# Optimization experiments

Hardware: AMD Instinct MI355X
Metric: run time of the kernel (lower is better)

Reference implementation:

```python
import jax, jax.numpy as jnp
import numpy as np

N = 50000          # nodes
E = 800000         # edges (avg degree 16)
IN, H, OUT = 128, 256, 128
K = 100            # low-rank attention rank (hard-coded self.k = 100)
BN_EPS = 1e-5


def _lin(key, din, dout):
    return jax.random.normal(key, (din, dout), jnp.float32) / np.sqrt(din)


def setup_inputs() -> dict:
    key = jax.random.key(0)
    ks = jax.random.split(key, 16)
    inp = {
        "x": jax.random.normal(ks[0], (N, IN), jnp.float32),
        "edge_index": jax.random.randint(ks[1], (2, E), 0, N, jnp.int32),
    }
    dins = [IN, H, H]
    douts = [H, H, OUT]
    j = 2
    for i, (di, do) in enumerate(zip(dins, douts)):
        inp[f"cw{i}"] = _lin(ks[j], di, H); j += 1          # GCNConv weight
        inp[f"cb{i}"] = jnp.zeros((H,), jnp.float32)          # GCNConv bias
        inp[f"aw{i}"] = _lin(ks[j], di, 4 * K); j += 1        # attention U|V|Z|T projection
        inp[f"ab{i}"] = jnp.zeros((4 * K,), jnp.float32)
        inp[f"rw{i}"] = _lin(ks[j], 2 * K + H, do); j += 1    # dimension_reduce linear
        inp[f"rb{i}"] = jnp.zeros((do,), jnp.float32)
    for i in range(2):                                        # BN for first num_layers-1 blocks
        inp[f"g{i}"] = jnp.ones((H,), jnp.float32)
        inp[f"bt{i}"] = jnp.zeros((H,), jnp.float32)
    return inp


def _gcn(x, W, b, src, dst):
    n = x.shape[0]
    loops = jnp.arange(n, dtype=src.dtype)
    s = jnp.concatenate([src, loops])
    d = jnp.concatenate([dst, loops])
    deg = jax.ops.segment_sum(jnp.ones(d.shape, x.dtype), d, num_segments=n)
    dis = jax.lax.rsqrt(jnp.maximum(deg, 1.0))  # deg >= 1 due to self loops
    h = x @ W                                    # [N, H]
    msg = h[s] * (dis[s] * dis[d])[:, None]      # [E+N, H]
    return jax.ops.segment_sum(msg, d, num_segments=n) + b


def _lowrank(x, Aw, Ab):
    # LowRankAttention: tmp = relu(x W); split into U,V,Z,T of width K each.
    t = jax.nn.relu(x @ Aw + Ab)                 # [N, 4K]
    U, V, Z, T = t[:, :K], t[:, K:2 * K], t[:, 2 * K:3 * K], t[:, 3 * K:]
    n = x.shape[0]
    # joint_normalize2: scalar norm factor
    nf = jnp.sum(U @ (V.T @ jnp.ones((n, 1), x.dtype))) / n + 1e-6
    res = U @ (V.T @ Z)                          # low-rank global attention [N, K]
    return jnp.concatenate([res / nf, T], axis=1)  # [N, 2K]


def _bn(x, g, b):
    m = jnp.mean(x, axis=0)
    v = jnp.var(x, axis=0)
    return (x - m) * jax.lax.rsqrt(v + BN_EPS) * g + b


def reference(x, edge_index, cw0, cb0, aw0, ab0, rw0, rb0, g0, bt0,
              cw1, cb1, aw1, ab1, rw1, rb1, g1, bt1,
              cw2, cb2, aw2, ab2, rw2, rb2):
    src, dst = edge_index[0], edge_index[1]
    layers = [(cw0, cb0, aw0, ab0, rw0, rb0, g0, bt0),
              (cw1, cb1, aw1, ab1, rw1, rb1, g1, bt1)]
    for cw, cb, aw, ab, rw, rb, g, bt in layers:
        x_local = jax.nn.relu(_gcn(x, cw, cb, src, dst))  # dropout p=0 (eval)
        x_global = _lowrank(x, aw, ab)
        x = jax.nn.relu(jnp.concatenate([x_global, x_local], axis=1) @ rw + rb)
        x = _bn(x, g, bt)
    x_local = jax.nn.relu(_gcn(x, cw2, cb2, src, dst))
    x_global = _lowrank(x, aw2, ab2)
    return jnp.concatenate([x_global, x_local], axis=1) @ rw2 + rb2
```

## Files before the change

### kernel.cpp

```cpp
#include <hip/hip_runtime.h>

typedef _Float16 f16;
typedef __attribute__((ext_vector_type(8))) _Float16 f16x8;
typedef __attribute__((ext_vector_type(4))) _Float16 f16x4;
typedef __attribute__((ext_vector_type(2))) _Float16 f16x2;
typedef __attribute__((ext_vector_type(4))) float f32x4;

#define BKMAX 256
#define LDB   264

__global__ __launch_bounds__(256, 2) void gemm_fused3(
    const f16* __restrict__ A, int lda,
    const f16* __restrict__ Bt, int Kd,
    const float* __restrict__ biascat,
    f16* __restrict__ hb, f16* __restrict__ tbuf, f16* __restrict__ xcatT,
    int R, float* __restrict__ csbuf)
{
    __shared__ f16 Bs[128 * LDB];
    const int tid  = threadIdx.x;
    const int wid  = tid >> 6;
    const int lane = tid & 63;
    const int m    = lane & 15;
    const int quad = lane >> 4;

    const long row0    = (long)blockIdx.x * 256 + wid * 64;
    const int  colbase = blockIdx.y * 128;

    f32x4 acc[4][8];
#pragma unroll
    for (int rt = 0; rt < 4; ++rt)
#pragma unroll
        for (int ct = 0; ct < 8; ++ct)
            acc[rt][ct] = f32x4{0.f, 0.f, 0.f, 0.f};

    const f16* Aptr[4];
#pragma unroll
    for (int rt = 0; rt < 4; ++rt) {
        long r = row0 + rt * 16 + m;
        if (r > (long)R - 1) r = (long)R - 1;
        Aptr[rt] = A + r * (long)lda + quad * 8;
    }
    f16x8 pa[4];
#pragma unroll
    for (int rt = 0; rt < 4; ++rt) pa[rt] = *(const f16x8*)(Aptr[rt]);

    const int  scol  = tid >> 1;
    const int  shalf = (tid & 1) * 8;
    const long sbase = (long)(colbase + scol) * Kd;

    for (int k0 = 0; k0 < Kd; k0 += BKMAX) {
        const int BK = (Kd - k0 < BKMAX) ? (Kd - k0) : BKMAX;
        if (k0 != 0) __syncthreads();
        for (int kc = shalf; kc < BK; kc += 16)
            *(f16x8*)&Bs[scol * LDB + kc] = *(const f16x8*)(Bt + sbase + k0 + kc);
        __syncthreads();
#pragma unroll 2
        for (int kk = 0; kk < BK; kk += 32) {
            f16x8 a[4];
#pragma unroll
            for (int rt = 0; rt < 4; ++rt) a[rt] = pa[rt];
            int kn = k0 + kk + 32;
            if (kn < Kd) {
#pragma unroll
                for (int rt = 0; rt < 4; ++rt) pa[rt] = *(const f16x8*)(Aptr[rt] + kn);
            }
#pragma unroll
            for (int ct = 0; ct < 8; ++ct) {
                f16x8 b = *(const f16x8*)&Bs[(ct * 16 + m) * LDB + kk + quad * 8];
#pragma unroll
                for (int rt = 0; rt < 4; ++rt)
                    acc[rt][ct] = __builtin_amdgcn_mfma_f32_16x16x32_f16(a[rt], b, acc[rt][ct], 0, 0, 0);
            }
        }
    }

    float rsum[8];
#pragma unroll
    for (int ct = 0; ct < 8; ++ct) rsum[ct] = 0.f;

#pragma unroll
    for (int ct = 0; ct < 8; ++ct) {
        int col = colbase + ct * 16 + m;
        if (col >= 656) continue;
        float bv = biascat[col];
        bool isrelu = col >= 256;
        f16* dst; int ldc2, c2;
        if (col < 256)      { dst = hb;    ldc2 = 256; c2 = col; }
        else if (col < 556) { dst = tbuf;  ldc2 = 300; c2 = col - 256; }
        else                { dst = xcatT; ldc2 = 456; c2 = col - 556; }
#pragma unroll
        for (int rt = 0; rt < 4; ++rt) {
#pragma unroll
            for (int r = 0; r < 4; ++r) {
                long row = row0 + rt * 16 + quad * 4 + r;
                if (row < R) {
                    float v = acc[rt][ct][r] + bv;
                    if (isrelu && v < 0.f) v = 0.f;
                    dst[row * (long)ldc2 + c2] = (f16)v;
                    rsum[ct] += v;
                }
            }
        }
    }

    if (colbase == 256 || colbase == 384) {
        __syncthreads();
        float* scr = (float*)Bs;
#pragma unroll
        for (int ct = 0; ct < 8; ++ct) {
            float s = rsum[ct];
            s += __shfl_xor(s, 16);
            s += __shfl_xor(s, 32);
            if (quad == 0) scr[wid * 128 + ct * 16 + m] = s;
        }
        __syncthreads();
        if (tid < 128) {
            int gcol = colbase + tid;
            if (gcol < 456) {
                float s = scr[tid] + scr[128 + tid] + scr[256 + tid] + scr[384 + tid];
                atomicAdd(&csbuf[gcol - 256], s);
            }
        }
    }
}

__global__ __launch_bounds__(256) void gemm_mfma(
    const f16* __restrict__ A, int lda,
    const f16* __restrict__ Bt, int Kd,
    const float* __restrict__ bias,
    f16* __restrict__ Cb, float* __restrict__ Cf, int ldc,
    int R, int ncols, int relu,
    const float* __restrict__ scale_ptr)
{
    __shared__ f16 Bs[128 * LDB];
    const int tid  = threadIdx.x;
    const int wid  = tid >> 6;
    const int lane = tid & 63;
    const int m    = lane & 15;
    const int quad = lane >> 4;

    const long row0    = (long)blockIdx.x * 128 + wid * 32;
    const int  colbase = blockIdx.y * 128;

    f32x4 acc[2][8];
#pragma unroll
    for (int rt = 0; rt < 2; ++rt)
#pragma unroll
        for (int ct = 0; ct < 8; ++ct)
            acc[rt][ct] = f32x4{0.f, 0.f, 0.f, 0.f};

    const f16* Aptr[2];
#pragma unroll
    for (int rt = 0; rt < 2; ++rt) {
        long r = row0 + rt * 16 + m;
        if (r > (long)R - 1) r = (long)R - 1;
        Aptr[rt] = A + r * (long)lda + quad * 8;
    }
    f16x8 pa0 = *(const f16x8*)(Aptr[0]);
    f16x8 pa1 = *(const f16x8*)(Aptr[1]);

    const int  scol  = tid >> 1;
    const int  shalf = (tid & 1) * 8;
    const long sbase = (long)(colbase + scol) * Kd;

    for (int k0 = 0; k0 < Kd; k0 += BKMAX) {
        const int BK = (Kd - k0 < BKMAX) ? (Kd - k0) : BKMAX;
        if (k0 != 0) __syncthreads();
        for (int kc = shalf; kc < BK; kc += 16)
            *(f16x8*)&Bs[scol * LDB + kc] = *(const f16x8*)(Bt + sbase + k0 + kc);
        __syncthreads();
#pragma unroll 2
        for (int kk = 0; kk < BK; kk += 32) {
            f16x8 a0 = pa0, a1 = pa1;
            int kn = k0 + kk + 32;
            if (kn < Kd) {
                pa0 = *(const f16x8*)(Aptr[0] + kn);
                pa1 = *(const f16x8*)(Aptr[1] + kn);
            }
#pragma unroll
            for (int ct = 0; ct < 8; ++ct) {
                f16x8 b = *(const f16x8*)&Bs[(ct * 16 + m) * LDB + kk + quad * 8];
                acc[0][ct] = __builtin_amdgcn_mfma_f32_16x16x32_f16(a0, b, acc[0][ct], 0, 0, 0);
                acc[1][ct] = __builtin_amdgcn_mfma_f32_16x16x32_f16(a1, b, acc[1][ct], 0, 0, 0);
            }
        }
    }

    const float scale = scale_ptr ? *scale_ptr : 1.f;
#pragma unroll
    for (int ct = 0; ct < 8; ++ct) {
        int col = colbase + ct * 16 + m;
        if (col >= ncols) continue;
        float bv = bias ? bias[col] : 0.f;
#pragma unroll
        for (int rt = 0; rt < 2; ++rt) {
#pragma unroll
            for (int r = 0; r < 4; ++r) {
                long row = row0 + rt * 16 + quad * 4 + r;
                if (row < R) {
                    float v = acc[rt][ct][r] * scale + bv;
                    if (relu && v < 0.f) v = 0.f;
                    if (Cf) Cf[row * (long)ldc + col] = v;
                    else    Cb[row * (long)ldc + col] = (f16)v;
                }
            }
        }
    }
}

__global__ __launch_bounds__(256, 2) void gemm_mfma_t(
    const f16* __restrict__ A, int lda,
    const f16* __restrict__ Bt, int Kd,
    const float* __restrict__ bias,
    f16* __restrict__ Cb, float* __restrict__ Cf, int ldc,
    int R, int ncols, int relu,
    float* __restrict__ bnsum_ptr)
{
    __shared__ f16 Bs[128 * LDB];
    const int tid  = threadIdx.x;
    const int wid  = tid >> 6;
    const int lane = tid & 63;
    const int m    = lane & 15;
    const int quad = lane >> 4;

    const long row0    = (long)blockIdx.x * 256 + wid * 64;
    const int  colbase = blockIdx.y * 128;

    f32x4 acc[4][8];
#pragma unroll
    for (int rt = 0; rt < 4; ++rt)
#pragma unroll
        for (int ct = 0; ct < 8; ++ct)
            acc[rt][ct] = f32x4{0.f, 0.f, 0.f, 0.f};

    const f16* Aptr[4];
#pragma unroll
    for (int rt = 0; rt < 4; ++rt) {
        long r = row0 + rt * 16 + m;
        if (r > (long)R - 1) r = (long)R - 1;
        Aptr[rt] = A + r * (long)lda + quad * 8;
    }
    f16x8 pa[4];
#pragma unroll
    for (int rt = 0; rt < 4; ++rt) pa[rt] = *(const f16x8*)(Aptr[rt]);

    const int  scol  = tid >> 1;
    const int  shalf = (tid & 1) * 8;
    const long sbase = (long)(colbase + scol) * Kd;

    for (int k0 = 0; k0 < Kd; k0 += BKMAX) {
        const int BK = (Kd - k0 < BKMAX) ? (Kd - k0) : BKMAX;
        if (k0 != 0) __syncthreads();
        for (int kc = shalf; kc < BK; kc += 16)
            *(f16x8*)&Bs[scol * LDB + kc] = *(const f16x8*)(Bt + sbase + k0 + kc);
        __syncthreads();
#pragma unroll 2
        for (int kk = 0; kk < BK; kk += 32) {
            f16x8 a[4];
#pragma unroll
            for (int rt = 0; rt < 4; ++rt) a[rt] = pa[rt];
            int kn = k0 + kk + 32;
            if (kn < Kd) {
#pragma unroll
                for (int rt = 0; rt < 4; ++rt) pa[rt] = *(const f16x8*)(Aptr[rt] + kn);
            }
#pragma unroll
            for (int ct = 0; ct < 8; ++ct) {
                f16x8 b = *(const f16x8*)&Bs[(ct * 16 + m) * LDB + kk + quad * 8];
#pragma unroll
                for (int rt = 0; rt < 4; ++rt)
                    acc[rt][ct] = __builtin_amdgcn_mfma_f32_16x16x32_f16(a[rt], b, acc[rt][ct], 0, 0, 0);
            }
        }
    }

    float rsum[8], rsq[8];
#pragma unroll
    for (int ct = 0; ct < 8; ++ct) { rsum[ct] = 0.f; rsq[ct] = 0.f; }

#pragma unroll
    for (int ct = 0; ct < 8; ++ct) {
        int col = colbase + ct * 16 + m;
        if (col >= ncols) continue;
        float bv = bias ? bias[col] : 0.f;
#pragma unroll
        for (int rt = 0; rt < 4; ++rt) {
#pragma unroll
            for (int r = 0; r < 4; ++r) {
                long row = row0 + rt * 16 + quad * 4 + r;
                if (row < R) {
                    float v = acc[rt][ct][r] + bv;
                    if (relu && v < 0.f) v = 0.f;
                    if (Cf) Cf[row * (long)ldc + col] = v;
                    else    Cb[row * (long)ldc + col] = (f16)v;
                    rsum[ct] += v;
                    rsq[ct]  += v * v;
                }
            }
        }
    }

    if (bnsum_ptr) {
        __syncthreads();
        float* scr = (float*)Bs;
#pragma unroll
        for (int ct = 0; ct < 8; ++ct) {
            float s = rsum[ct];
            s += __shfl_xor(s, 16);
            s += __shfl_xor(s, 32);
            float q = rsq[ct];
            q += __shfl_xor(q, 16);
            q += __shfl_xor(q, 32);
            if (quad == 0) {
                scr[wid * 128 + ct * 16 + m]       = s;
                scr[512 + wid * 128 + ct * 16 + m] = q;
            }
        }
        __syncthreads();
        if (tid < 128) {
            int col = colbase + tid;
            if (col < ncols) {
                float s = scr[tid] + scr[128 + tid] + scr[256 + tid] + scr[384 + tid];
                float q = scr[512 + tid] + scr[640 + tid] + scr[768 + tid] + scr[896 + tid];
                atomicAdd(&bnsum_ptr[col], s);
                atomicAdd(&bnsum_ptr[256 + col], q);
            }
        }
    }
}

struct PrepJobs {
    const float* src[13];
    void*        dst[13];
    int   K[13], ncols[13], Kd[13], type[13];
    long  start[13], elems[13];
    int   njobs;
};

__global__ __launch_bounds__(256) void prep_all(PrepJobs J)
{
    long b = blockIdx.x;
    int j = 0;
    for (int i = 1; i < J.njobs; ++i)
        if (b >= J.start[i]) j = i;
    long idx = (b - J.start[j]) * 256 + threadIdx.x;
    if (idx >= J.elems[j]) return;
    int ty = J.type[j];
    if (ty == 0) {
        int Kd = J.Kd[j];
        int k = (int)(idx % Kd);
        long n = idx / Kd;
        float v = (k < J.K[j] && n < J.ncols[j]) ? J.src[j][(long)k * J.ncols[j] + n] : 0.f;
        ((f16*)J.dst[j])[idx] = (f16)v;
    } else if (ty == 1) {
        ((f16*)J.dst[j])[idx] = (f16)J.src[j][idx];
    } else if (ty == 2) {
        ((float*)J.dst[j])[idx] = 0.f;
    } else {
        float v = (idx >= 256 && idx < 656) ? J.src[j][idx - 256] : 0.f;
        ((float*)J.dst[j])[idx] = v;
    }
}

__global__ void hist_kernel(const int* __restrict__ dst, int E, int* __restrict__ cnt)
{
    int e = blockIdx.x * 256 + threadIdx.x;
    if (e < E) atomicAdd(&cnt[dst[e]], 1);
}

__global__ __launch_bounds__(1024) void scanA_kernel(const int* __restrict__ cnt, int n,
                                                     int* __restrict__ csum)
{
    __shared__ int sdata[1024];
    int t = threadIdx.x;
    int i = blockIdx.x * 1024 + t;
    sdata[t] = (i < n) ? cnt[i] : 0;
    __syncthreads();
    for (int d = 512; d > 0; d >>= 1) {
        if (t < d) sdata[t] += sdata[t + d];
        __syncthreads();
    }
    if (t == 0) csum[blockIdx.x] = sdata[0];
}

__global__ void scanB_kernel(int* __restrict__ csum, int nchunks, int n, int* __restrict__ rowptr)
{
    if (threadIdx.x == 0) {
        int run = 0;
        for (int b = 0; b < nchunks; ++b) {
            int v = csum[b];
            csum[b] = run;
            run += v;
        }
        rowptr[n] = run;
    }
}

__global__ __launch_bounds__(1024) void scanC_kernel(const int* __restrict__ cnt, int n,
                                                     const int* __restrict__ csum,
                                                     int* __restrict__ rowptr,
                                                     int* __restrict__ cursor,
                                                     float* __restrict__ dis)
{
    __shared__ int sdata[1024];
    int t = threadIdx.x;
    int i = blockIdx.x * 1024 + t;
    int v = (i < n) ? cnt[i] : 0;
    sdata[t] = v;
    __syncthreads();
    for (int d = 1; d < 1024; d <<= 1) {
        int x = (t >= d) ? sdata[t - d] : 0;
        __syncthreads();
        sdata[t] += x;
        __syncthreads();
    }
    if (i < n) {
        int excl = csum[blockIdx.x] + sdata[t] - v;
        rowptr[i] = excl;
        cursor[i] = excl;
        dis[i] = rsqrtf((float)(v + 1));
    }
}

__global__ void scatter_kernel(const int* __restrict__ src, const int* __restrict__ dst,
                               int E, int* __restrict__ cursor, int* __restrict__ colidx)
{
    int e = blockIdx.x * 256 + threadIdx.x;
    if (e < E) {
        int d = dst[e];
        int pos = atomicAdd(&cursor[d], 1);
        colidx[pos] = src[e];
    }
}

__global__ __launch_bounds__(256) void agg_kernel(
    const f16* __restrict__ h, const int* __restrict__ rowptr,
    const int* __restrict__ colidx, const float* __restrict__ dis,
    const float* __restrict__ cb, f16* __restrict__ out, int ldc, int R)
{
    int wid = threadIdx.x >> 6, lane = threadIdx.x & 63;
    int i = blockIdx.x * 4 + wid;
    if (i >= R) return;
    float disi = dis[i];
    f16x4 hv = *(const f16x4*)(h + (long)i * 256 + lane * 4);
    float acc[4];
#pragma unroll
    for (int j = 0; j < 4; ++j) acc[j] = (float)hv[j] * disi;
    int e0 = rowptr[i], e1 = rowptr[i + 1];
    int e = e0;
    for (; e + 3 < e1; e += 4) {
        int s0 = colidx[e], s1 = colidx[e + 1], s2 = colidx[e + 2], s3 = colidx[e + 3];
        float w0 = dis[s0], w1 = dis[s1], w2 = dis[s2], w3 = dis[s3];
        f16x4 h0 = *(const f16x4*)(h + (long)s0 * 256 + lane * 4);
        f16x4 h1 = *(const f16x4*)(h + (long)s1 * 256 + lane * 4);
        f16x4 h2 = *(const f16x4*)(h + (long)s2 * 256 + lane * 4);
        f16x4 h3 = *(const f16x4*)(h + (long)s3 * 256 + lane * 4);
#pragma unroll
        for (int j = 0; j < 4; ++j)
            acc[j] += (float)h0[j] * w0 + (float)h1[j] * w1
                    + (float)h2[j] * w2 + (float)h3[j] * w3;
    }
    for (; e < e1; ++e) {
        int s = colidx[e];
        float w = dis[s];
        f16x4 hs = *(const f16x4*)(h + (long)s * 256 + lane * 4);
#pragma unroll
        for (int j = 0; j < 4; ++j) acc[j] += (float)hs[j] * w;
    }
    f16x4 o;
#pragma unroll
    for (int j = 0; j < 4; ++j) {
        float v = acc[j] * disi + cb[lane * 4 + j];
        if (v < 0.f) v = 0.f;
        o[j] = (f16)v;
    }
    *(f16x4*)(out + (long)i * ldc + lane * 4) = o;
}

#define VTZ_BLOCKS 192
__global__ __launch_bounds__(256) void vtz_mfma(const f16* __restrict__ t, int ld, int R,
                                                float* __restrict__ Mpart)
{
    __shared__ f16 Vt[112 * 72];
    __shared__ f16 Zt[112 * 72];
    const int tid  = threadIdx.x;
    const int wid  = tid >> 6;
    const int lane = tid & 63;
    const int m    = lane & 15;
    const int quad = lane >> 4;

    for (int idx = tid; idx < 12 * 64; idx += 256) {
        int c = 100 + (idx >> 6), r = idx & 63;
        Vt[c * 72 + r] = (f16)0.f;
        Zt[c * 72 + r] = (f16)0.f;
    }

    f32x4 acc[2][7];
#pragma unroll
    for (int rt = 0; rt < 2; ++rt)
#pragma unroll
        for (int ct = 0; ct < 7; ++ct)
            acc[rt][ct] = f32x4{0.f, 0.f, 0.f, 0.f};

    for (long base = (long)blockIdx.x * 64; base < R; base += (long)gridDim.x * 64) {
        __syncthreads();
        for (int idx = tid; idx < 50 * 64; idx += 256) {
            int r = idx / 50, c2 = (idx - r * 50) * 2;
            f16x2 v2 = f16x2{(f16)0.f, (f16)0.f};
            f16x2 z2 = f16x2{(f16)0.f, (f16)0.f};
            if (base + r < R) {
                v2 = *(const f16x2*)(t + (base + r) * ld + 100 + c2);
                z2 = *(const f16x2*)(t + (base + r) * ld + 200 + c2);
            }
            Vt[c2 * 72 + r] = v2[0]; Vt[(c2 + 1) * 72 + r] = v2[1];
            Zt[c2 * 72 + r] = z2[0]; Zt[(c2 + 1) * 72 + r] = z2[1];
        }
        __syncthreads();
#pragma unroll
        for (int ks = 0; ks < 2; ++ks) {
            int k0 = ks * 32 + quad * 8;
            f16x8 b[7];
#pragma unroll
            for (int ct = 0; ct < 7; ++ct)
                b[ct] = *(const f16x8*)&Zt[(ct * 16 + m) * 72 + k0];
#pragma unroll
            for (int rt = 0; rt < 2; ++rt) {
                int tr = wid + rt * 4;
                if (tr >= 7) continue;
                f16x8 a = *(const f16x8*)&Vt[(tr * 16 + m) * 72 + k0];
#pragma unroll
                for (int ct = 0; ct < 7; ++ct)
                    acc[rt][ct] = __builtin_amdgcn_mfma_f32_16x16x32_f16(a, b[ct], acc[rt][ct], 0, 0, 0);
            }
        }
    }

    float* out = Mpart + (long)blockIdx.x * 10000;
#pragma unroll
    for (int rt = 0; rt < 2; ++rt) {
        int tr = wid + rt * 4;
        if (tr >= 7) continue;
#pragma unroll
        for (int ct = 0; ct < 7; ++ct) {
            int b = ct * 16 + m;
            if (b >= 100) continue;
#pragma unroll
            for (int r = 0; r < 4; ++r) {
                int a = tr * 16 + quad * 4 + r;
                if (a < 100) out[a * 100 + b] = acc[rt][ct][r];
            }
        }
    }
}

__global__ __launch_bounds__(256) void vtz_reduce2(const float* __restrict__ Mpart,
                                                   f16* __restrict__ MT,
                                                   const float* __restrict__ cs, int R)
{
    __shared__ float s2[256];
    int t = threadIdx.x;
    float v = (t < 100) ? cs[t] * cs[100 + t] : 0.f;
    s2[t] = v;
    __syncthreads();
    for (int d = 128; d > 0; d >>= 1) {
        if (t < d) s2[t] += s2[t + d];
        __syncthreads();
    }
    float scale = 1.0f / (s2[0] / (float)R + 1e-6f);

    int idx = blockIdx.x * 256 + t;
    if (idx >= 10000) return;
    float s = 0.f;
    for (int b = 0; b < VTZ_BLOCKS; ++b) s += Mpart[(long)b * 10000 + idx];
    s *= scale;
    int a = idx / 100, c = idx - a * 100;
    MT[c * 128 + a] = (f16)s;
}

__global__ __launch_bounds__(256) void bn_fold2(
    f16* __restrict__ bigBT,
    const float* __restrict__ cwf, const float* __restrict__ awf,
    const float* __restrict__ bnsum, const float* __restrict__ g,
    const float* __restrict__ bt, int R,
    const float* __restrict__ ab0, float* __restrict__ biascat)
{
    __shared__ float a_s[256], b_s[256];
    const int t = threadIdx.x;
    {
        float s0 = bnsum[t];
        float s1 = bnsum[256 + t];
        float mean = s0 / (float)R;
        float var  = s1 / (float)R - mean * mean;
        if (var < 0.f) var = 0.f;
        float a = g[t] * rsqrtf(var + 1e-5f);
        a_s[t] = a;
        b_s[t] = bt[t] - mean * a;
    }
    __syncthreads();
    const int bid = blockIdx.x;
    if (bid < 768) {
        long idx = (long)bid * 256 + t;
        bigBT[idx] = (f16)((float)bigBT[idx] * a_s[t]);
    } else if (bid == 768) {
        float s = 0.f;
        for (int k = 0; k < 256; ++k) s += b_s[k] * cwf[(long)k * 256 + t];
        biascat[t] = s;
    } else {
        int n = (bid - 769) * 256 + t;
        if (n < 400) {
            float s = ab0[n];
            for (int k = 0; k < 256; ++k) s += b_s[k] * awf[(long)k * 400 + n];
            biascat[256 + n] = s;
        }
    }
}

extern "C" void kernel_launch(void* const* d_in, const int* in_sizes, int n_in,
                              void* d_out, int out_size, void* d_ws, size_t ws_size,
                              hipStream_t stream)
{
    (void)n_in; (void)out_size; (void)ws_size;
    const int N = in_sizes[0] / 128;
    const int E = in_sizes[1] / 2;

    const float* x0 = (const float*)d_in[0];
    const int*  ei   = (const int*)d_in[1];
    const int*  esrc = ei;
    const int*  edst = ei + E;
    const float *cw[3], *cbv[3], *aw[3], *abv[3], *rw[3], *rbv[3];
    for (int l = 0; l < 3; ++l) {
        cw[l]  = (const float*)d_in[2 + 6 * l];
        cbv[l] = (const float*)d_in[3 + 6 * l];
        aw[l]  = (const float*)d_in[4 + 6 * l];
        abv[l] = (const float*)d_in[5 + 6 * l];
        rw[l]  = (const float*)d_in[6 + 6 * l];
        rbv[l] = (const float*)d_in[7 + 6 * l];
    }
    const float* g[2]   = {(const float*)d_in[20], (const float*)d_in[22]};
    const float* btb[2] = {(const float*)d_in[21], (const float*)d_in[23]};

    char* p = (char*)d_ws;
    auto carve = [&](size_t bytes) -> char* {
        char* r = p; p += (bytes + 255) & ~(size_t)255; return r;
    };
    int*   cnt    = (int*)carve((size_t)N * 4);
    int*   rowptr = (int*)carve((size_t)(N + 1) * 4);
    int*   cursor = (int*)carve((size_t)N * 4);
    int*   colidx = (int*)carve((size_t)E * 4);
    float* dis    = (float*)carve((size_t)N * 4);
    int*   csum   = (int*)carve(256 * 4);
    float* Mpart  = (float*)carve((size_t)VTZ_BLOCKS * 10000 * 4);
    float* zr     = (float*)carve(9984 * 4);
    float* csbufL[3] = {zr, zr + 256, zr + 512};
    float* bnsumA = zr + 768;
    float* bnsumB = zr + 1280;
    f16*   MT     = (f16*)(zr + 1792);
    float* biascat = (float*)carve(768 * 4);
    f16*   bigBT[3], *rwT[3];
    int din[3] = {128, 256, 256};
    int dou[3] = {256, 256, 128};
    for (int l = 0; l < 3; ++l) {
        bigBT[l] = (f16*)carve((size_t)768 * din[l] * 2);
        rwT[l]   = (f16*)carve((size_t)dou[l] * 480 * 2);
    }
    f16*   xbf  = (f16*)carve((size_t)N * 256 * 2);
    float* hbuf = (float*)carve((size_t)N * 256 * 4);
    f16*   hb   = (f16*)hbuf;
    f16*   tbuf = (f16*)carve((size_t)N * 300 * 2);
    f16*   xcat = (f16*)carve(((size_t)N * 456 + 32) * 2);

    PrepJobs J{};
    int nj = 0; long blk = 0;
    auto addJob = [&](const float* s, void* d, int K, int nc, int Kd, int ty, long elems) {
        J.src[nj] = s; J.dst[nj] = d; J.K[nj] = K; J.ncols[nj] = nc; J.Kd[nj] = Kd;
        J.type[nj] = ty; J.start[nj] = blk; J.elems[nj] = elems;
        blk += (elems + 255) / 256; ++nj;
    };
    for (int l = 0; l < 3; ++l)
        addJob(cw[l], bigBT[l], din[l], 256, din[l], 0, (long)256 * din[l]);
    for (int l = 0; l < 3; ++l)
        addJob(aw[l], bigBT[l] + (long)256 * din[l], din[l], 400, din[l], 0, (long)512 * din[l]);
    for (int l = 0; l < 3; ++l)
        addJob(rw[l], rwT[l], 456, dou[l], 480, 0, (long)dou[l] * 480);
    addJob(x0, xbf, 0, 0, 0, 1, (long)N * 128);
    addJob(nullptr, zr, 0, 0, 0, 2, 9984);
    addJob(nullptr, cnt, 0, 0, 0, 2, N);
    addJob(abv[0], biascat, 0, 0, 0, 3, 768);
    J.njobs = nj;

    prep_all<<<(unsigned)blk, 256, 0, stream>>>(J);

    const int nchunks = (N + 1023) / 1024;
    hist_kernel<<<(E + 255) / 256, 256, 0, stream>>>(edst, E, cnt);
    scanA_kernel<<<nchunks, 1024, 0, stream>>>(cnt, N, csum);
    scanB_kernel<<<1, 64, 0, stream>>>(csum, nchunks, N, rowptr);
    scanC_kernel<<<nchunks, 1024, 0, stream>>>(cnt, N, csum, rowptr, cursor, dis);
    scatter_kernel<<<(E + 255) / 256, 256, 0, stream>>>(esrc, edst, E, cursor, colidx);

    int lda = 128;
    const unsigned gx  = (unsigned)((N + 127) / 128);
    const unsigned gx2 = (unsigned)((N + 255) / 256);

    for (int l = 0; l < 3; ++l) {
        float* bnsumX = (l == 0) ? bnsumA : bnsumB;

        gemm_fused3<<<dim3(gx2, 6), 256, 0, stream>>>(xbf, lda, bigBT[l], din[l], biascat,
                                                      hb, tbuf, xcat + 100, N, csbufL[l]);
        vtz_mfma<<<VTZ_BLOCKS, 256, 0, stream>>>(tbuf, 300, N, Mpart);
        vtz_reduce2<<<40, 256, 0, stream>>>(Mpart, MT, csbufL[l], N);
        gemm_mfma<<<dim3(gx, 1), 256, 0, stream>>>(tbuf, 300, MT, 128, nullptr,
                                                   xcat, nullptr, 456, N, 100, 0, nullptr);
        agg_kernel<<<(N + 3) / 4, 256, 0, stream>>>(hb, rowptr, colidx, dis, cbv[l],
                                                    xcat + 200, 456, N);
        if (l < 2) {
            gemm_mfma_t<<<dim3(gx2, 2), 256, 0, stream>>>(xcat, 456, rwT[l], 480, rbv[l],
                                                          xbf, nullptr, 256, N, 256, 1,
                                                          bnsumX);
            bn_fold2<<<771, 256, 0, stream>>>(bigBT[l + 1], cw[l + 1], aw[l + 1],
                                              bnsumX, g[l], btb[l], N,
                                              abv[l + 1], biascat);
            lda = 256;
        } else {
            gemm_mfma<<<dim3(gx, 1), 256, 0, stream>>>(xcat, 456, rwT[l], 480, rbv[l],
                                                       nullptr, (float*)d_out, 128, N, 128, 0, nullptr);
        }
    }
}
```

Measured before the change: 957.6 us.

## Unify GEMMs into one kernel staging both A and B tiles in LDS

Replaces three GEMM kernels with a single templated-by-mode kernel that stages 256x64 A tiles and 128x64 B tiles into shared memory per k-step, instead of streaming A directly from global with register prefetch and staging full-K B tiles. The smaller tiles (row stride 72) cut LDS use, which should let two blocks fit per CU, and A rows are now loaded cooperatively and coalesced. The narrow GEMMs also move from 128-row to 256-row tiles. In exchange the global-load prefetch overlap is lost and there are more syncs per K.

Result: slower. 980.2 us (+2.4%).

```diff
diff --git a/kernel.cpp b/kernel.cpp
--- a/kernel.cpp
+++ b/kernel.cpp
@@ -6,24 +6,29 @@
 typedef __attribute__((ext_vector_type(2))) _Float16 f16x2;
 typedef __attribute__((ext_vector_type(4))) float f32x4;
 
-#define BKMAX 256
-#define LDB   264
-
-__global__ __launch_bounds__(256, 2) void gemm_fused3(
+#define LDA2 72
+
+__global__ __launch_bounds__(256, 2) void gemm2(
     const f16* __restrict__ A, int lda,
     const f16* __restrict__ Bt, int Kd,
-    const float* __restrict__ biascat,
-    f16* __restrict__ hb, f16* __restrict__ tbuf, f16* __restrict__ xcatT,
-    int R, float* __restrict__ csbuf)
-{
-    __shared__ f16 Bs[128 * LDB];
+    const float* __restrict__ bias,
+    f16* __restrict__ Cb, float* __restrict__ Cf, int ldc,
+    int R, int ncols, int relu,
+    float* __restrict__ csbuf,
+    float* __restrict__ bnsum_ptr,
+    f16* __restrict__ hbD, f16* __restrict__ tbufD, f16* __restrict__ xcatD,
+    int mode)
+{
+    __shared__ f16 As[256 * LDA2];
+    __shared__ f16 Bs[128 * LDA2];
     const int tid  = threadIdx.x;
     const int wid  = tid >> 6;
     const int lane = tid & 63;
     const int m    = lane & 15;
     const int quad = lane >> 4;
 
-    const long row0    = (long)blockIdx.x * 256 + wid * 64;
+    const long rowblk = (long)blockIdx.x * 256;
+    const long row0   = rowblk + wid * 64;
     const int  colbase = blockIdx.y * 128;
 
     f32x4 acc[4][8];
@@ -33,297 +38,138 @@
         for (int ct = 0; ct < 8; ++ct)
             acc[rt][ct] = f32x4{0.f, 0.f, 0.f, 0.f};
 
-    const f16* Aptr[4];
-#pragma unroll
-    for (int rt = 0; rt < 4; ++rt) {
-        long r = row0 + rt * 16 + m;
-        if (r > (long)R - 1) r = (long)R - 1;
-        Aptr[rt] = A + r * (long)lda + quad * 8;
-    }
-    f16x8 pa[4];
-#pragma unroll
-    for (int rt = 0; rt < 4; ++rt) pa[rt] = *(const f16x8*)(Aptr[rt]);
-
-    const int  scol  = tid >> 1;
-    const int  shalf = (tid & 1) * 8;
-    const long sbase = (long)(colbase + scol) * Kd;
-
-    for (int k0 = 0; k0 < Kd; k0 += BKMAX) {
-        const int BK = (Kd - k0 < BKMAX) ? (Kd - k0) : BKMAX;
-        if (k0 != 0) __syncthreads();
-        for (int kc = shalf; kc < BK; kc += 16)
-            *(f16x8*)&Bs[scol * LDB + kc] = *(const f16x8*)(Bt + sbase + k0 + kc);
+    for (int k0 = 0; k0 < Kd; k0 += 64) {
+        const int BK = (Kd - k0 >= 64) ? 64 : (Kd - k0);
+        const int sb = (BK == 64) ? 3 : 2;
+        const int smask = (1 << sb) - 1;
+        if (k0) __syncthreads();
+        const int itA = BK >> 3;
+        for (int i = 0; i < itA; ++i) {
+            int u = i * 256 + tid;
+            int r = u >> sb, s = u & smask;
+            long rr = rowblk + r; if (rr > (long)R - 1) rr = (long)R - 1;
+            *(f16x8*)&As[r * LDA2 + s * 8] = *(const f16x8*)(A + rr * (long)lda + k0 + s * 8);
+        }
+        const int itB = BK >> 4;
+        for (int i = 0; i < itB; ++i) {
+            int u = i * 256 + tid;
+            int c = u >> sb, s = u & smask;
+            *(f16x8*)&Bs[c * LDA2 + s * 8] =
+                *(const f16x8*)(Bt + (long)(colbase + c) * Kd + k0 + s * 8);
+        }
         __syncthreads();
 #pragma unroll 2
         for (int kk = 0; kk < BK; kk += 32) {
-            f16x8 a[4];
-#pragma unroll
-            for (int rt = 0; rt < 4; ++rt) a[rt] = pa[rt];
-            int kn = k0 + kk + 32;
-            if (kn < Kd) {
-#pragma unroll
-                for (int rt = 0; rt < 4; ++rt) pa[rt] = *(const f16x8*)(Aptr[rt] + kn);
-            }
+            f16x8 a[4], b[8];
+#pragma unroll
+            for (int rt = 0; rt < 4; ++rt)
+                a[rt] = *(const f16x8*)&As[(wid * 64 + rt * 16 + m) * LDA2 + kk + quad * 8];
+#pragma unroll
+            for (int ct = 0; ct < 8; ++ct)
+                b[ct] = *(const f16x8*)&Bs[(ct * 16 + m) * LDA2 + kk + quad * 8];
+#pragma unroll
+            for (int ct = 0; ct < 8; ++ct)
+#pragma unroll
+                for (int rt = 0; rt < 4; ++rt)
+                    acc[rt][ct] = __builtin_amdgcn_mfma_f32_16x16x32_f16(a[rt], b[ct], acc[rt][ct], 0, 0, 0);
+        }
+    }
+
+    float rsum[8], rsq[8];
+#pragma unroll
+    for (int ct = 0; ct < 8; ++ct) { rsum[ct] = 0.f; rsq[ct] = 0.f; }
+
+    if (mode == 1) {
+#pragma unroll
+        for (int ct = 0; ct < 8; ++ct) {
+            int col = colbase + ct * 16 + m;
+            if (col >= 656) continue;
+            float bv = bias[col];
+            bool isrelu = col >= 256;
+            f16* dst; int ldc2, c2;
+            if (col < 256)      { dst = hbD;   ldc2 = 256; c2 = col; }
+            else if (col < 556) { dst = tbufD; ldc2 = 300; c2 = col - 256; }
+            else                { dst = xcatD; ldc2 = 456; c2 = col - 556; }
+#pragma unroll
+            for (int rt = 0; rt < 4; ++rt) {
+#pragma unroll
+                for (int r = 0; r < 4; ++r) {
+                    long row = row0 + rt * 16 + quad * 4 + r;
+                    if (row < R) {
+                        float v = acc[rt][ct][r] + bv;
+                        if (isrelu && v < 0.f) v = 0.f;
+                        dst[row * (long)ldc2 + c2] = (f16)v;
+                        rsum[ct] += v;
+                    }
+                }
+            }
+        }
+        if (colbase == 256 || colbase == 384) {
+            __syncthreads();
+            float* scr = (float*)Bs;
 #pragma unroll
             for (int ct = 0; ct < 8; ++ct) {
-                f16x8 b = *(const f16x8*)&Bs[(ct * 16 + m) * LDB + kk + quad * 8];
-#pragma unroll
-                for (int rt = 0; rt < 4; ++rt)
-                    acc[rt][ct] = __builtin_amdgcn_mfma_f32_16x16x32_f16(a[rt], b, acc[rt][ct], 0, 0, 0);
-            }
-        }
-    }
-
-    float rsum[8];
-#pragma unroll
-    for (int ct = 0; ct < 8; ++ct) rsum[ct] = 0.f;
-
-#pragma unroll
-    for (int ct = 0; ct < 8; ++ct) {
-        int col = colbase + ct * 16 + m;
-        if (col >= 656) continue;
-        float bv = biascat[col];
-        bool isrelu = col >= 256;
-        f16* dst; int ldc2, c2;
-        if (col < 256)      { dst = hb;    ldc2 = 256; c2 = col; }
-        else if (col < 556) { dst = tbuf;  ldc2 = 300; c2 = col - 256; }
-        else                { dst = xcatT; ldc2 = 456; c2 = col - 556; }
-#pragma unroll
-        for (int rt = 0; rt < 4; ++rt) {
-#pragma unroll
-            for (int r = 0; r < 4; ++r) {
-                long row = row0 + rt * 16 + quad * 4 + r;
-                if (row < R) {
-                    float v = acc[rt][ct][r] + bv;
-                    if (isrelu && v < 0.f) v = 0.f;
-                    dst[row * (long)ldc2 + c2] = (f16)v;
-                    rsum[ct] += v;
+                float s = rsum[ct];
+                s += __shfl_xor(s, 16);
+                s += __shfl_xor(s, 32);
+                if (quad == 0) scr[wid * 128 + ct * 16 + m] = s;
+            }
+            __syncthreads();
+            if (tid < 128) {
+                int gcol = colbase + tid;
+                if (gcol < 456) {
+                    float s = scr[tid] + scr[128 + tid] + scr[256 + tid] + scr[384 + tid];
+                    atomicAdd(&csbuf[gcol - 256], s);
                 }
             }
         }
-    }
-
-    if (colbase == 256 || colbase == 384) {
-        __syncthreads();
-        float* scr = (float*)Bs;
+    } else {
 #pragma unroll
         for (int ct = 0; ct < 8; ++ct) {
-            float s = rsum[ct];
-            s += __shfl_xor(s, 16);
-            s += __shfl_xor(s, 32);
-            if (quad == 0) scr[wid * 128 + ct * 16 + m] = s;
-        }
-        __syncthreads();
-        if (tid < 128) {
-            int gcol = colbase + tid;
-            if (gcol < 456) {
-                float s = scr[tid] + scr[128 + tid] + scr[256 + tid] + scr[384 + tid];
-                atomicAdd(&csbuf[gcol - 256], s);
-            }
-        }
-    }
-}
-
-__global__ __launch_bounds__(256) void gemm_mfma(
-    const f16* __restrict__ A, int lda,
-    const f16* __restrict__ Bt, int Kd,
-    const float* __restrict__ bias,
-    f16* __restrict__ Cb, float* __restrict__ Cf, int ldc,
-    int R, int ncols, int relu,
-    const float* __restrict__ scale_ptr)
-{
-    __shared__ f16 Bs[128 * LDB];
-    const int tid  = threadIdx.x;
-    const int wid  = tid >> 6;
-    const int lane = tid & 63;
-    const int m    = lane & 15;
-    const int quad = lane >> 4;
-
-    const long row0    = (long)blockIdx.x * 128 + wid * 32;
-    const int  colbase = blockIdx.y * 128;
-
-    f32x4 acc[2][8];
-#pragma unroll
-    for (int rt = 0; rt < 2; ++rt)
-#pragma unroll
-        for (int ct = 0; ct < 8; ++ct)
-            acc[rt][ct] = f32x4{0.f, 0.f, 0.f, 0.f};
-
-    const f16* Aptr[2];
-#pragma unroll
-    for (int rt = 0; rt < 2; ++rt) {
-        long r = row0 + rt * 16 + m;
-        if (r > (long)R - 1) r = (long)R - 1;
-        Aptr[rt] = A + r * (long)lda + quad * 8;
-    }
-    f16x8 pa0 = *(const f16x8*)(Aptr[0]);
-    f16x8 pa1 = *(const f16x8*)(Aptr[1]);
-
-    const int  scol  = tid >> 1;
-    const int  shalf = (tid & 1) * 8;
-    const long sbase = (long)(colbase + scol) * Kd;
-
-    for (int k0 = 0; k0 < Kd; k0 += BKMAX) {
-        const int BK = (Kd - k0 < BKMAX) ? (Kd - k0) : BKMAX;
-        if (k0 != 0) __syncthreads();
-        for (int kc = shalf; kc < BK; kc += 16)
-            *(f16x8*)&Bs[scol * LDB + kc] = *(const f16x8*)(Bt + sbase + k0 + kc);
-        __syncthreads();
-#pragma unroll 2
-        for (int kk = 0; kk < BK; kk += 32) {
-            f16x8 a0 = pa0, a1 = pa1;
-            int kn = k0 + kk + 32;
-            if (kn < Kd) {
-                pa0 = *(const f16x8*)(Aptr[0] + kn);
-                pa1 = *(const f16x8*)(Aptr[1] + kn);
-            }
+            int col = colbase + ct * 16 + m;
+            if (col >= ncols) continue;
+            float bv = bias ? bias[col] : 0.f;
+#pragma unroll
+            for (int rt = 0; rt < 4; ++rt) {
+#pragma unroll
+                for (int r = 0; r < 4; ++r) {
+                    long row = row0 + rt * 16 + quad * 4 + r;
+                    if (row < R) {
+                        float v = acc[rt][ct][r] + bv;
+                        if (relu && v < 0.f) v = 0.f;
+                        if (Cf) Cf[row * (long)ldc + col] = v;
+                        else    Cb[row * (long)ldc + col] = (f16)v;
+                        rsum[ct] += v;
+                        rsq[ct]  += v * v;
+                    }
+                }
+            }
+        }
+        if (bnsum_ptr) {
+            __syncthreads();
+            float* scr = (float*)Bs;
 #pragma unroll
             for (int ct = 0; ct < 8; ++ct) {
-                f16x8 b = *(const f16x8*)&Bs[(ct * 16 + m) * LDB + kk + quad * 8];
-                acc[0][ct] = __builtin_amdgcn_mfma_f32_16x16x32_f16(a0, b, acc[0][ct], 0, 0, 0);
-                acc[1][ct] = __builtin_amdgcn_mfma_f32_16x16x32_f16(a1, b, acc[1][ct], 0, 0, 0);
-            }
-        }
-    }
-
-    const float scale = scale_ptr ? *scale_ptr : 1.f;
-#pragma unroll
-    for (int ct = 0; ct < 8; ++ct) {
-        int col = colbase + ct * 16 + m;
-        if (col >= ncols) continue;
-        float bv = bias ? bias[col] : 0.f;
-#pragma unroll
-        for (int rt = 0; rt < 2; ++rt) {
-#pragma unroll
-            for (int r = 0; r < 4; ++r) {
-                long row = row0 + rt * 16 + quad * 4 + r;
-                if (row < R) {
-                    float v = acc[rt][ct][r] * scale + bv;
-                    if (relu && v < 0.f) v = 0.f;
-                    if (Cf) Cf[row * (long)ldc + col] = v;
-                    else    Cb[row * (long)ldc + col] = (f16)v;
+                float s = rsum[ct];
+                s += __shfl_xor(s, 16);
+                s += __shfl_xor(s, 32);
+                float q = rsq[ct];
+                q += __shfl_xor(q, 16);
+                q += __shfl_xor(q, 32);
+                if (quad == 0) {
+                    scr[wid * 128 + ct * 16 + m]       = s;
+                    scr[512 + wid * 128 + ct * 16 + m] = q;
                 }
             }
-        }
-    }
-}
-
-__global__ __launch_bounds__(256, 2) void gemm_mfma_t(
-    const f16* __restrict__ A, int lda,
-    const f16* __restrict__ Bt, int Kd,
-    const float* __restrict__ bias,
-    f16* __restrict__ Cb, float* __restrict__ Cf, int ldc,
-    int R, int ncols, int relu,
-    float* __restrict__ bnsum_ptr)
-{
-    __shared__ f16 Bs[128 * LDB];
-    const int tid  = threadIdx.x;
-    const int wid  = tid >> 6;
-    const int lane = tid & 63;
-    const int m    = lane & 15;
-    const int quad = lane >> 4;
-
-    const long row0    = (long)blockIdx.x * 256 + wid * 64;
-    const int  colbase = blockIdx.y * 128;
-
-    f32x4 acc[4][8];
-#pragma unroll
-    for (int rt = 0; rt < 4; ++rt)
-#pragma unroll
-        for (int ct = 0; ct < 8; ++ct)
-            acc[rt][ct] = f32x4{0.f, 0.f, 0.f, 0.f};
-
-    const f16* Aptr[4];
-#pragma unroll
-    for (int rt = 0; rt < 4; ++rt) {
-        long r = row0 + rt * 16 + m;
-        if (r > (long)R - 1) r = (long)R - 1;
-        Aptr[rt] = A + r * (long)lda + quad * 8;
-    }
-    f16x8 pa[4];
-#pragma unroll
-    for (int rt = 0; rt < 4; ++rt) pa[rt] = *(const f16x8*)(Aptr[rt]);
-
-    const int  scol  = tid >> 1;
-    const int  shalf = (tid & 1) * 8;
-    const long sbase = (long)(colbase + scol) * Kd;
-
-    for (int k0 = 0; k0 < Kd; k0 += BKMAX) {
-        const int BK = (Kd - k0 < BKMAX) ? (Kd - k0) : BKMAX;
-        if (k0 != 0) __syncthreads();
-        for (int kc = shalf; kc < BK; kc += 16)
-            *(f16x8*)&Bs[scol * LDB + kc] = *(const f16x8*)(Bt + sbase + k0 + kc);
-        __syncthreads();
-#pragma unroll 2
-        for (int kk = 0; kk < BK; kk += 32) {
-            f16x8 a[4];
-#pragma unroll
-            for (int rt = 0; rt < 4; ++rt) a[rt] = pa[rt];
-            int kn = k0 + kk + 32;
-            if (kn < Kd) {
-#pragma unroll
-                for (int rt = 0; rt < 4; ++rt) pa[rt] = *(const f16x8*)(Aptr[rt] + kn);
-            }
-#pragma unroll
-            for (int ct = 0; ct < 8; ++ct) {
-                f16x8 b = *(const f16x8*)&Bs[(ct * 16 + m) * LDB + kk + quad * 8];
-#pragma unroll
-                for (int rt = 0; rt < 4; ++rt)
-                    acc[rt][ct] = __builtin_amdgcn_mfma_f32_16x16x32_f16(a[rt], b, acc[rt][ct], 0, 0, 0);
-            }
-        }
-    }
-
-    float rsum[8], rsq[8];
-#pragma unroll
-    for (int ct = 0; ct < 8; ++ct) { rsum[ct] = 0.f; rsq[ct] = 0.f; }
-
-#pragma unroll
-    for (int ct = 0; ct < 8; ++ct) {
-        int col = colbase + ct * 16 + m;
-        if (col >= ncols) continue;
-        float bv = bias ? bias[col] : 0.f;
-#pragma unroll
-        for (int rt = 0; rt < 4; ++rt) {
-#pragma unroll
-            for (int r = 0; r < 4; ++r) {
-                long row = row0 + rt * 16 + quad * 4 + r;
-                if (row < R) {
-                    float v = acc[rt][ct][r] + bv;
-                    if (relu && v < 0.f) v = 0.f;
-                    if (Cf) Cf[row * (long)ldc + col] = v;
-                    else    Cb[row * (long)ldc + col] = (f16)v;
-                    rsum[ct] += v;
-                    rsq[ct]  += v * v;
+            __syncthreads();
+            if (tid < 128) {
+                int col = colbase + tid;
+                if (col < ncols) {
+                    float s = scr[tid] + scr[128 + tid] + scr[256 + tid] + scr[384 + tid];
+                    float q = scr[512 + tid] + scr[640 + tid] + scr[768 + tid] + scr[896 + tid];
+                    atomicAdd(&bnsum_ptr[col], s);
+                    atomicAdd(&bnsum_ptr[256 + col], q);
                 }
-            }
-        }
-    }
-
-    if (bnsum_ptr) {
-        __syncthreads();
-        float* scr = (float*)Bs;
-#pragma unroll
-        for (int ct = 0; ct < 8; ++ct) {
-            float s = rsum[ct];
-            s += __shfl_xor(s, 16);
-            s += __shfl_xor(s, 32);
-            float q = rsq[ct];
-            q += __shfl_xor(q, 16);
-            q += __shfl_xor(q, 32);
-            if (quad == 0) {
-                scr[wid * 128 + ct * 16 + m]       = s;
-                scr[512 + wid * 128 + ct * 16 + m] = q;
-            }
-        }
-        __syncthreads();
-        if (tid < 128) {
-            int col = colbase + tid;
-            if (col < ncols) {
-                float s = scr[tid] + scr[128 + tid] + scr[256 + tid] + scr[384 + tid];
-                float q = scr[512 + tid] + scr[640 + tid] + scr[768 + tid] + scr[896 + tid];
-                atomicAdd(&bnsum_ptr[col], s);
-                atomicAdd(&bnsum_ptr[256 + col], q);
             }
         }
     }
@@ -698,31 +544,37 @@
     scatter_kernel<<<(E + 255) / 256, 256, 0, stream>>>(esrc, edst, E, cursor, colidx);
 
     int lda = 128;
-    const unsigned gx  = (unsigned)((N + 127) / 128);
     const unsigned gx2 = (unsigned)((N + 255) / 256);
 
     for (int l = 0; l < 3; ++l) {
         float* bnsumX = (l == 0) ? bnsumA : bnsumB;
 
-        gemm_fused3<<<dim3(gx2, 6), 256, 0, stream>>>(xbf, lda, bigBT[l], din[l], biascat,
-                                                      hb, tbuf, xcat + 100, N, csbufL[l]);
+        gemm2<<<dim3(gx2, 6), 256, 0, stream>>>(xbf, lda, bigBT[l], din[l], biascat,
+                                                nullptr, nullptr, 0, N, 656, 0,
+                                                csbufL[l], nullptr,
+                                                hb, tbuf, xcat + 100, 1);
         vtz_mfma<<<VTZ_BLOCKS, 256, 0, stream>>>(tbuf, 300, N, Mpart);
         vtz_reduce2<<<40, 256, 0, stream>>>(Mpart, MT, csbufL[l], N);
-        gemm_mfma<<<dim3(gx, 1), 256, 0, stream>>>(tbuf, 300, MT, 128, nullptr,
-                                                   xcat, nullptr, 456, N, 100, 0, nullptr);
+        gemm2<<<dim3(gx2, 1), 256, 0, stream>>>(tbuf, 300, MT, 128, nullptr,
+                                                xcat, nullptr, 456, N, 100, 0,
+                                                nullptr, nullptr,
+                                                nullptr, nullptr, nullptr, 0);
         agg_kernel<<<(N + 3) / 4, 256, 0, stream>>>(hb, rowptr, colidx, dis, cbv[l],
                                                     xcat + 200, 456, N);
         if (l < 2) {
-            gemm_mfma_t<<<dim3(gx2, 2), 256, 0, stream>>>(xcat, 456, rwT[l], 480, rbv[l],
-                                                          xbf, nullptr, 256, N, 256, 1,
-                                                          bnsumX);
+            gemm2<<<dim3(gx2, 2), 256, 0, stream>>>(xcat, 456, rwT[l], 480, rbv[l],
+                                                    xbf, nullptr, 256, N, 256, 1,
+                                                    nullptr, bnsumX,
+                                                    nullptr, nullptr, nullptr, 0);
             bn_fold2<<<771, 256, 0, stream>>>(bigBT[l + 1], cw[l + 1], aw[l + 1],
                                               bnsumX, g[l], btb[l], N,
                                               abv[l + 1], biascat);
             lda = 256;
         } else {
-            gemm_mfma<<<dim3(gx, 1), 256, 0, stream>>>(xcat, 456, rwT[l], 480, rbv[l],
-                                                       nullptr, (float*)d_out, 128, N, 128, 0, nullptr);
-        }
-    }
-}
+            gemm2<<<dim3(gx2, 1), 256, 0, stream>>>(xcat, 456, rwT[l], 480, rbv[l],
+                                                    nullptr, (float*)d_out, 128, N, 128, 0,
+                                                    nullptr, nullptr,
+                                                    nullptr, nullptr, nullptr, 0);
+        }
+    }
+}
```
